# Optimization experiments

Hardware: AMD Instinct MI355X
Metric: run time of the kernel (lower is better)

The kernel has to match this reference:

```python
import jax, jax.numpy as jnp
import numpy as np

N = 32768   # nodes
E = 524288  # edges (avg degree 16)
F = 32      # num_features
H = 512     # hidden_channels
C = 10      # num_classes
G = 64      # graphs in batch


def setup_inputs() -> dict:
    key = jax.random.key(0)
    ks = jax.random.split(key, 16)
    s = 0.05  # weight init scale
    f32 = jnp.float32
    return {
        "x": jax.random.normal(ks[0], (N, F), f32),
        "edge_index": jax.random.randint(ks[1], (2, E), 0, N),
        "batch_index": jnp.sort(jax.random.randint(ks[2], (N,), 0, G)),
        # initial_conv: F -> H  (PyG GraphConv: lin_root on x, lin_rel on aggregated neighbors)
        "w_root0": jax.random.normal(ks[3], (F, H), f32) * s,
        "w_rel0": jax.random.normal(ks[4], (F, H), f32) * s,
        "b0": jnp.zeros((H,), f32),
        # conv1..conv4 stacked: H -> H
        "w_root": jax.random.normal(ks[5], (4, H, H), f32) * s,
        "w_rel": jax.random.normal(ks[6], (4, H, H), f32) * s,
        "b": jnp.zeros((4, H), f32),
        # MLP tail
        "lin1_w": jax.random.normal(ks[7], (2 * H, H), f32) * s,
        "lin1_b": jnp.zeros((H,), f32),
        "lin2_w": jax.random.normal(ks[8], (H, H), f32) * s,
        "lin2_b": jnp.zeros((H,), f32),
        "lin3_w": jax.random.normal(ks[9], (H, C), f32) * s,
        "lin3_b": jnp.zeros((C,), f32),
    }


def _graph_conv(h, src, dst, w_root, w_rel, bias):
    # out_i = h_i @ W_root + (sum_{j->i} h_j) @ W_rel + b   (PyG GraphConv, aggr='add')
    agg = jax.ops.segment_sum(h[src], dst, num_segments=N)
    return h @ w_root + agg @ w_rel + bias


def reference(x, edge_index, batch_index,
              w_root0, w_rel0, b0, w_root, w_rel, b,
              lin1_w, lin1_b, lin2_w, lin2_b, lin3_w, lin3_b):
    src, dst = edge_index[0], edge_index[1]
    h = jnp.tanh(_graph_conv(x, src, dst, w_root0, w_rel0, b0))
    for i in range(4):  # fixed small layer loop
        h = jnp.tanh(_graph_conv(h, src, dst, w_root[i], w_rel[i], b[i]))
    # global max + mean pool over graphs
    gmax = jax.ops.segment_max(h, batch_index, num_segments=G)
    gsum = jax.ops.segment_sum(h, batch_index, num_segments=G)
    cnt = jax.ops.segment_sum(jnp.ones((N,), h.dtype), batch_index, num_segments=G)
    gmean = gsum / jnp.maximum(cnt, 1.0)[:, None]
    g = jnp.concatenate([gmax, gmean], axis=1)  # [G, 2H]
    # dropout is identity at inference (training=False)
    g = jnp.tanh(g @ lin1_w + lin1_b)
    g = jnp.tanh(g @ lin2_w + lin2_b)
    logits = g @ lin3_w + lin3_b
    return jax.nn.log_softmax(logits, axis=1)
```

## Files before the change

### kernel.cpp

```cpp
#include <hip/hip_runtime.h>
#include <hip/hip_bf16.h>
#include <math.h>

#define NN 32768
#define EE 524288
#define FF 32
#define HH 512
#define GG 64
#define CC 10

typedef __attribute__((ext_vector_type(8))) short short8;
typedef __attribute__((ext_vector_type(4))) float floatx4;
typedef __attribute__((ext_vector_type(4))) unsigned int uintx4;

__device__ __forceinline__ float bf16_to_f32(unsigned short u) {
    union { unsigned int u; float f; } v;
    v.u = ((unsigned int)u) << 16;
    return v.f;
}
__device__ __forceinline__ unsigned short f32_to_bf16(float f) {
    union { float f; unsigned int u; } v;
    v.f = f;
    unsigned int u = v.u;
    u += 0x7FFFu + ((u >> 16) & 1u);
    return (unsigned short)(u >> 16);
}
__device__ __forceinline__ float fast_tanh(float x) {
    float e = __expf(2.0f * x);
    return 1.0f - 2.0f * __builtin_amdgcn_rcpf(e + 1.0f);
}

__global__ __launch_bounds__(256) void prep_all_kernel(const float* __restrict__ wr0, const float* __restrict__ wl0,
                                unsigned short* __restrict__ WT0,
                                const float* __restrict__ wroot, const float* __restrict__ wrel,
                                unsigned short* __restrict__ WTs,
                                const float* __restrict__ x, unsigned short* __restrict__ X0) {
    const int b = blockIdx.x;
    const int tid = threadIdx.x;
    if (b < 520) {
        __shared__ unsigned short tile[64][65];
        const int ty = tid >> 6, tx = tid & 63;
        if (b < 8) {
            const int n0 = b * 64;
#pragma unroll
            for (int q = 0; q < 16; ++q) {
                const int k = ty * 16 + q;
                const float v = (k < 32) ? wr0[k * 512 + n0 + tx]
                                         : wl0[(k - 32) * 512 + n0 + tx];
                tile[k][tx] = f32_to_bf16(v);
            }
            __syncthreads();
#pragma unroll
            for (int q = 0; q < 16; ++q) {
                const int n = n0 + ty * 16 + q;
                WT0[n * 64 + tx] = tile[tx][ty * 16 + q];
            }
        } else {
            const int bb = b - 8;
            const int l = bb >> 7;
            const int r = bb & 127;
            const int k0 = (r >> 3) * 64;
            const int n0 = (r & 7) * 64;
            const float* Wl = (k0 < 512) ? wroot + (size_t)l * 262144
                                         : wrel + (size_t)l * 262144;
            const int kb = (k0 < 512) ? k0 : k0 - 512;
#pragma unroll
            for (int q = 0; q < 16; ++q) {
                const int kk = ty * 16 + q;
                tile[kk][tx] = f32_to_bf16(Wl[(size_t)(kb + kk) * 512 + n0 + tx]);
            }
            __syncthreads();
#pragma unroll
            for (int q = 0; q < 16; ++q) {
                const int n = n0 + ty * 16 + q;
                WTs[(size_t)l * 524288 + (size_t)n * 1024 + k0 + tx] = tile[tx][ty * 16 + q];
            }
        }
    } else {
        const int t = (b - 520) * 256 + tid;
        const int i = t >> 5, c = t & 31;
        X0[(size_t)i * 64 + c] = f32_to_bf16(x[t]);
    }
}

__global__ void zero_i32(int* __restrict__ p, int n) {
    int i = blockIdx.x * blockDim.x + threadIdx.x;
    if (i < n) p[i] = 0;
}
__global__ void hist_kernel(const int* __restrict__ dst, int* __restrict__ counts) {
    int e = blockIdx.x * blockDim.x + threadIdx.x;
    if (e < EE) atomicAdd(&counts[dst[e]], 1);
}
__global__ __launch_bounds__(1024) void scan_kernel(const int* __restrict__ counts,
                                                    int* __restrict__ rowStart,
                                                    int* __restrict__ cursor) {
    __shared__ int part[1024];
    const int t = threadIdx.x;
    const int base = t * 32;
    int local[32];
    const int4* cp = (const int4*)(counts + base);
    int s = 0;
#pragma unroll
    for (int ii = 0; ii < 8; ++ii) {
        int4 v = cp[ii];
        local[ii * 4 + 0] = v.x; local[ii * 4 + 1] = v.y;
        local[ii * 4 + 2] = v.z; local[ii * 4 + 3] = v.w;
        s += v.x + v.y + v.z + v.w;
    }
    part[t] = s;
    __syncthreads();
    for (int off = 1; off < 1024; off <<= 1) {
        int v = (t >= off) ? part[t - off] : 0;
        __syncthreads();
        part[t] += v;
        __syncthreads();
    }
    int run = part[t] - s;
#pragma unroll
    for (int i = 0; i < 32; ++i) {
        rowStart[base + i] = run;
        cursor[base + i] = run;
        run += local[i];
    }
    if (t == 1023) rowStart[NN] = run;
}
__global__ void scatter_kernel(const int* __restrict__ src, const int* __restrict__ dst,
                               int* __restrict__ cursor, int* __restrict__ ssrc) {
    int e = blockIdx.x * blockDim.x + threadIdx.x;
    if (e < EE) {
        int p = atomicAdd(&cursor[dst[e]], 1);
        ssrc[p] = src[e];
    }
}
__global__ __launch_bounds__(256) void deg_hist_kernel(const int* __restrict__ counts,
                                                       int* __restrict__ degHist) {
    __shared__ int lh[256];
    lh[threadIdx.x] = 0;
    __syncthreads();
    int i = blockIdx.x * 256 + threadIdx.x;
    int d = counts[i]; if (d > 255) d = 255;
    atomicAdd(&lh[255 - d], 1);
    __syncthreads();
    int v = lh[threadIdx.x];
    if (v) atomicAdd(&degHist[threadIdx.x], v);
}
__global__ __launch_bounds__(256) void deg_scan_kernel(const int* __restrict__ degHist,
                                                       int* __restrict__ degCursor) {
    __shared__ int sh[256];
    const int t = threadIdx.x;
    int own = degHist[t];
    sh[t] = own;
    __syncthreads();
    for (int off = 1; off < 256; off <<= 1) {
        int v = (t >= off) ? sh[t - off] : 0;
        __syncthreads();
        sh[t] += v;
        __syncthreads();
    }
    degCursor[t] = sh[t] - own;
}
__global__ __launch_bounds__(256) void deg_scatter_kernel(const int* __restrict__ counts,
                                                          int* __restrict__ degCursor,
                                                          int* __restrict__ perm,
                                                          int* __restrict__ pDeg) {
    __shared__ int lh[256];
    __shared__ int base[256];
    lh[threadIdx.x] = 0;
    __syncthreads();
    int i = blockIdx.x * 256 + threadIdx.x;
    int dtrue = counts[i];
    int d = dtrue > 255 ? 255 : dtrue;
    int bin = 255 - d;
    int lr = atomicAdd(&lh[bin], 1);
    __syncthreads();
    int c = lh[threadIdx.x];
    if (c) base[threadIdx.x] = atomicAdd(&degCursor[threadIdx.x], c);
    __syncthreads();
    int p = base[bin] + lr;
    perm[p] = i;
    pDeg[p] = dtrue;
}
__global__ __launch_bounds__(256) void edge_copy_kernel(const int* __restrict__ rowStart,
                                                        const int* __restrict__ perm,
                                                        const int* __restrict__ pRowStart,
                                                        const int* __restrict__ ssrc,
                                                        int* __restrict__ pssrc) {
    const int wv = threadIdx.x >> 6, lane = threadIdx.x & 63;
    const int sub = lane >> 4, l16 = lane & 15;
    const int p = blockIdx.x * 16 + wv * 4 + sub;
    const int node = perm[p];
    const int s = rowStart[node], e = rowStart[node + 1];
    const int ns = pRowStart[p];
    for (int j = s + l16; j < e; j += 16) pssrc[ns + (j - s)] = ssrc[j];
}

__device__ __forceinline__ void acc8(float* a, uint4 d) {
    a[0] += bf16_to_f32((unsigned short)(d.x & 0xFFFFu));
    a[1] += bf16_to_f32((unsigned short)(d.x >> 16));
    a[2] += bf16_to_f32((unsigned short)(d.y & 0xFFFFu));
    a[3] += bf16_to_f32((unsigned short)(d.y >> 16));
    a[4] += bf16_to_f32((unsigned short)(d.z & 0xFFFFu));
    a[5] += bf16_to_f32((unsigned short)(d.z >> 16));
    a[6] += bf16_to_f32((unsigned short)(d.w & 0xFFFFu));
    a[7] += bf16_to_f32((unsigned short)(d.w >> 16));
}
__device__ __forceinline__ void acc8v(float* a, uintx4 d) {
    a[0] += bf16_to_f32((unsigned short)(d[0] & 0xFFFFu));
    a[1] += bf16_to_f32((unsigned short)(d[0] >> 16));
    a[2] += bf16_to_f32((unsigned short)(d[1] & 0xFFFFu));
    a[3] += bf16_to_f32((unsigned short)(d[1] >> 16));
    a[4] += bf16_to_f32((unsigned short)(d[2] & 0xFFFFu));
    a[5] += bf16_to_f32((unsigned short)(d[2] >> 16));
    a[6] += bf16_to_f32((unsigned short)(d[3] & 0xFFFFu));
    a[7] += bf16_to_f32((unsigned short)(d[3] >> 16));
}

__global__ __launch_bounds__(256) void agg_kernel(const unsigned short* __restrict__ Xh, int ldh,
                                                  int cols, unsigned short* __restrict__ Xagg,
                                                  int ldagg, const int* __restrict__ rowStart,
                                                  const int* __restrict__ ssrc) {
    const int node = blockIdx.x * 64 + (threadIdx.x >> 2);
    const int lc = threadIdx.x & 3;
    const int s = rowStart[node];
    const int e = rowStart[node + 1];
    float a[8] = {0.f, 0.f, 0.f, 0.f, 0.f, 0.f, 0.f, 0.f};
    const unsigned short* base = Xh + lc * 8;
    int i = s;
    for (; i + 4 <= e; i += 4) {
        int j0 = ssrc[i], j1 = ssrc[i + 1], j2 = ssrc[i + 2], j3 = ssrc[i + 3];
        uint4 d0 = *(const uint4*)(base + (size_t)j0 * 64);
        uint4 d1 = *(const uint4*)(base + (size_t)j1 * 64);
        uint4 d2 = *(const uint4*)(base + (size_t)j2 * 64);
        uint4 d3 = *(const uint4*)(base + (size_t)j3 * 64);
        acc8(a, d0); acc8(a, d1); acc8(a, d2); acc8(a, d3);
    }
    for (; i < e; ++i) {
        int j = ssrc[i];
        uint4 d = *(const uint4*)(base + (size_t)j * 64);
        acc8(a, d);
    }
    unsigned short* out = Xagg + (size_t)node * 64 + lc * 8;
#pragma unroll
    for (int c = 0; c < 8; ++c) out[c] = f32_to_bf16(a[c]);
}

#define GLOAD(dreg, voff) \
    asm volatile("buffer_load_dwordx4 %0, %1, %2, 0 offen" \
                 : "=v"(dreg) : "v"(voff), "s"(srsrc))

__global__ __launch_bounds__(256, 3) void agg_slice_kernel(const unsigned short* __restrict__ Xh,
                                                           unsigned short* __restrict__ Xagg,
                                                           const int* __restrict__ pRowStart,
                                                           const int* __restrict__ pssrc,
                                                           const int* __restrict__ perm) {
    const int slice = blockIdx.x & 7;
    const int pair = blockIdx.x >> 3;
    const int wv = threadIdx.x >> 6;
    const int lane = threadIdx.x & 63;
    const int ln = lane >> 3;
    const int lc = lane & 7;
    const int colOff = slice * 64 + lc * 8;
    const unsigned short* base = Xh + colOff;
    uintx4 srsrc;
    {
        union { const unsigned short* p; unsigned int u[2]; } ba;
        ba.p = Xh + slice * 64;
        srsrc[0] = ba.u[0];
        srsrc[1] = ba.u[1] & 0xFFFFu;
        srsrc[2] = 0xFFFFFFFFu;
        srsrc[3] = 0x00020000u;
    }
    const unsigned int lcoff = (unsigned int)(lc << 4);
#pragma unroll
    for (int half = 0; half < 2; ++half) {
        const int nb = half ? (1023 - pair) : pair;
        const int p = nb * 32 + wv * 8 + ln;
        const int node = perm[p];
        const int s = pRowStart[p];
        const int e = pRowStart[p + 1];
        float a[8] = {0.f, 0.f, 0.f, 0.f, 0.f, 0.f, 0.f, 0.f};
        int i = s;
        for (; i + 16 <= e; i += 16) {
            unsigned int vo[16];
#pragma unroll
            for (int u = 0; u < 16; ++u)
                vo[u] = (((unsigned int)pssrc[i + u]) << 11) | lcoff;
            uintx4 d0, d1, d2, d3, d4, d5, d6, d7, d8, d9, d10, d11, d12, d13, d14, d15;
            __builtin_amdgcn_sched_barrier(0);
            GLOAD(d0, vo[0]);   GLOAD(d1, vo[1]);   GLOAD(d2, vo[2]);   GLOAD(d3, vo[3]);
            GLOAD(d4, vo[4]);   GLOAD(d5, vo[5]);   GLOAD(d6, vo[6]);   GLOAD(d7, vo[7]);
            GLOAD(d8, vo[8]);   GLOAD(d9, vo[9]);   GLOAD(d10, vo[10]); GLOAD(d11, vo[11]);
            GLOAD(d12, vo[12]); GLOAD(d13, vo[13]); GLOAD(d14, vo[14]); GLOAD(d15, vo[15]);
            asm volatile("s_waitcnt vmcnt(8)" ::: "memory");
            __builtin_amdgcn_sched_barrier(0);
            acc8v(a, d0); acc8v(a, d1); acc8v(a, d2); acc8v(a, d3);
            acc8v(a, d4); acc8v(a, d5); acc8v(a, d6); acc8v(a, d7);
            asm volatile("s_waitcnt vmcnt(0)" ::: "memory");
            __builtin_amdgcn_sched_barrier(0);
            acc8v(a, d8);  acc8v(a, d9);  acc8v(a, d10); acc8v(a, d11);
            acc8v(a, d12); acc8v(a, d13); acc8v(a, d14); acc8v(a, d15);
        }
        if (e - i >= 8) {
            unsigned int vo[8];
#pragma unroll
            for (int u = 0; u < 8; ++u)
                vo[u] = (((unsigned int)pssrc[i + u]) << 11) | lcoff;
            uintx4 d0, d1, d2, d3, d4, d5, d6, d7;
            __builtin_amdgcn_sched_barrier(0);
            GLOAD(d0, vo[0]); GLOAD(d1, vo[1]); GLOAD(d2, vo[2]); GLOAD(d3, vo[3]);
            GLOAD(d4, vo[4]); GLOAD(d5, vo[5]); GLOAD(d6, vo[6]); GLOAD(d7, vo[7]);
            asm volatile("s_waitcnt vmcnt(4)" ::: "memory");
            __builtin_amdgcn_sched_barrier(0);
            acc8v(a, d0); acc8v(a, d1); acc8v(a, d2); acc8v(a, d3);
            asm volatile("s_waitcnt vmcnt(0)" ::: "memory");
            __builtin_amdgcn_sched_barrier(0);
            acc8v(a, d4); acc8v(a, d5); acc8v(a, d6); acc8v(a, d7);
            i += 8;
        }
        for (; i + 4 <= e; i += 4) {
            int j0 = pssrc[i], j1 = pssrc[i + 1], j2 = pssrc[i + 2], j3 = pssrc[i + 3];
            uint4 e0 = *(const uint4*)(base + (size_t)j0 * 1024);
            uint4 e1 = *(const uint4*)(base + (size_t)j1 * 1024);
            uint4 e2 = *(const uint4*)(base + (size_t)j2 * 1024);
            uint4 e3 = *(const uint4*)(base + (size_t)j3 * 1024);
            acc8(a, e0); acc8(a, e1); acc8(a, e2); acc8(a, e3);
        }
        for (; i < e; ++i) {
            int j = pssrc[i];
            uint4 d = *(const uint4*)(base + (size_t)j * 1024);
            acc8(a, d);
        }
        unsigned short* out = Xagg + (size_t)node * 1024 + colOff;
#pragma unroll
        for (int c = 0; c < 8; ++c) out[c] = f32_to_bf16(a[c]);
    }
}

__global__ __launch_bounds__(256, 4) void gemm_bias_tanh(const unsigned short* __restrict__ Xin,
                                                         int ldin, int K,
                                                         const unsigned short* __restrict__ WT,
                                                         const float* __restrict__ bias,
                                                         unsigned short* __restrict__ Xout,
                                                         int ldout) {
    __shared__ __align__(16) unsigned short As[128 * 64];
    __shared__ __align__(16) unsigned short Bs[128 * 64];
    const int tid = threadIdx.x;
    const int lane = tid & 63;
    const int wave = tid >> 6;
    const int wm = wave >> 1, wn = wave & 1;
    const int bm = blockIdx.x, bn = blockIdx.y;

    floatx4 acc[4][4] = {};

    const int lrow = lane >> 3;
    const int schunk = (lane & 7) ^ (lrow & 7);
    const unsigned short* Abase = Xin + (size_t)(bm * 128) * ldin;
    const unsigned short* Bbase = WT + (size_t)(bn * 128) * K;
    const int m = lane & 15;
    const int quad = lane >> 4;

    for (int k0 = 0; k0 < K; k0 += 64) {
        __syncthreads();
#pragma unroll
        for (int q = 0; q < 4; ++q) {
            const int rr = q * 32 + wave * 8;
            const int row = rr + lrow;
            const unsigned short* sa = Abase + (size_t)row * ldin + (k0 + schunk * 8);
            const unsigned short* sb = Bbase + (size_t)row * K + (k0 + schunk * 8);
            __builtin_amdgcn_global_load_lds(
                (const __attribute__((address_space(1))) void*)sa,
                (__attribute__((address_space(3))) void*)(&As[rr * 64]), 16, 0, 0);
            __builtin_amdgcn_global_load_lds(
                (const __attribute__((address_space(1))) void*)sb,
                (__attribute__((address_space(3))) void*)(&Bs[rr * 64]), 16, 0, 0);
        }
        __syncthreads();
#pragma unroll
        for (int half = 0; half < 2; ++half) {
            short8 af[4], bfr[4];
#pragma unroll
            for (int t = 0; t < 4; ++t) {
                const int row = wm * 64 + t * 16 + m;
                const int chunk = (half * 4 + quad) ^ (row & 7);
                af[t] = *(const short8*)&As[row * 64 + chunk * 8];
            }
#pragma unroll
            for (int t = 0; t < 4; ++t) {
                const int row = wn * 64 + t * 16 + m;
                const int chunk = (half * 4 + quad) ^ (row & 7);
                bfr[t] = *(const short8*)&Bs[row * 64 + chunk * 8];
            }
#pragma unroll
            for (int mt = 0; mt < 4; ++mt)
#pragma unroll
                for (int nt = 0; nt < 4; ++nt)
                    acc[mt][nt] = __builtin_amdgcn_mfma_f32_16x16x32_bf16(af[mt], bfr[nt],
                                                                          acc[mt][nt], 0, 0, 0);
        }
    }

    const int row0 = bm * 128 + wm * 64;
    const int col0 = bn * 128 + wn * 64;
#pragma unroll
    for (int mt = 0; mt < 4; ++mt) {
#pragma unroll
        for (int nt = 0; nt < 4; ++nt) {
            const int col = col0 + nt * 16 + m;
            const float bv = bias[col];
#pragma unroll
            for (int r = 0; r < 4; ++r) {
                const int row = row0 + mt * 16 + quad * 4 + r;
                float v = fast_tanh(acc[mt][nt][r] + bv);
                Xout[(size_t)row * ldout + col] = f32_to_bf16(v);
            }
        }
    }
}

__device__ __forceinline__ void stage_half(const unsigned short* __restrict__ gsrc0,
                                           int ldg, unsigned short* ldsHalf,
                                           int w, int lane) {
#pragma unroll
    for (int q = 0; q < 2; ++q) {
        const int rb = q * 64 + w * 8;
        const unsigned short* src = gsrc0 + (size_t)(rb + (lane >> 3)) * ldg
                                    + ((lane & 7) ^ (lane >> 3)) * 8;
        __builtin_amdgcn_global_load_lds(
            (const __attribute__((address_space(1))) void*)src,
            (__attribute__((address_space(3))) void*)(ldsHalf + rb * 64), 16, 0, 0);
    }
}
__device__ __forceinline__ void stage_q(const unsigned short* __restrict__ gsrc0,
                                        int ldg, unsigned short* ldsQ,
                                        int w, int lane) {
    const unsigned short* src = gsrc0 + (size_t)(w * 8 + (lane >> 3)) * ldg
                                + ((lane & 7) ^ (lane >> 3)) * 8;
    __builtin_amdgcn_global_load_lds(
        (const __attribute__((address_space(1))) void*)src,
        (__attribute__((address_space(3))) void*)(ldsQ + (w * 8) * 64), 16, 0, 0);
}

__global__ __launch_bounds__(512, 2) void gemm256_bias_tanh(
    const unsigned short* __restrict__ Xin, int ldin, int K,
    const unsigned short* __restrict__ WT, const float* __restrict__ bias,
    unsigned short* __restrict__ Xout, int ldout) {
    __shared__ __align__(16) unsigned short As[2][256 * 64];
    __shared__ __align__(16) unsigned short Bs[2][256 * 64];
    const int tid = threadIdx.x;
    const int lane = tid & 63;
    const int w = tid >> 6;
    const int wm = w >> 2, wn = w & 3;
    const int m = lane & 15, quad = lane >> 4;
    const int id = (int)blockIdx.x;
    const int bm = (id & 7) * 16 + (id >> 4);
    const int bn = (id >> 3) & 1;
    const int NT = K >> 6;

    const unsigned short* Abase = Xin + (size_t)(bm * 256) * ldin;
    const unsigned short* Bbase = WT + (size_t)(bn * 256) * K;

    floatx4 acc[8][4] = {};

#define STG_AH(buf, h, kt_) stage_half(Abase + (size_t)((h) * 128) * ldin + (kt_) * 64, ldin, \
                                       &As[buf][(h) * 128 * 64], w, lane)
#define STG_BH(buf, h, kt_) stage_half(Bbase + (size_t)((h) * 128) * K + (kt_) * 64, K, \
                                       &Bs[buf][(h) * 128 * 64], w, lane)
#define STG_AQ(buf, qr, kt_) stage_q(Abase + (size_t)((qr) * 64) * ldin + (kt_) * 64, ldin, \
                                     &As[buf][(qr) * 64 * 64], w, lane)

    STG_BH(0, 0, 0); STG_BH(0, 1, 0); STG_AH(0, 0, 0); STG_AH(0, 1, 0);
    STG_BH(1, 0, 1); STG_BH(1, 1, 1); STG_AH(1, 0, 1); STG_AH(1, 1, 1);
    asm volatile("s_waitcnt vmcnt(8)" ::: "memory");
    __builtin_amdgcn_s_barrier();

    for (int kt = 0; kt < NT; ++kt) {
        const int cur = kt & 1;
        const unsigned short* Ac = &As[cur][0];
        const unsigned short* Bc = &Bs[cur][0];
        const bool pf = (kt + 2 < NT);
        short8 afr[8], bfr[8];

#pragma unroll
        for (int nf = 0; nf < 4; ++nf)
#pragma unroll
            for (int ks = 0; ks < 2; ++ks) {
                const int col = wn * 64 + nf * 16 + m;
                const int chunk = (ks * 4 + quad) ^ (col & 7);
                bfr[nf * 2 + ks] = *(const short8*)&Bc[col * 64 + chunk * 8];
            }
#pragma unroll
        for (int t = 0; t < 4; ++t)
#pragma unroll
            for (int ks = 0; ks < 2; ++ks) {
                const int row = wm * 128 + t * 16 + m;
                const int chunk = (ks * 4 + quad) ^ (row & 7);
                afr[t * 2 + ks] = *(const short8*)&Ac[row * 64 + chunk * 8];
            }
        __builtin_amdgcn_s_barrier();
        __builtin_amdgcn_s_setprio(1);
#pragma unroll
        for (int t = 0; t < 4; ++t)
#pragma unroll
            for (int u = 0; u < 2; ++u)
#pragma unroll
                for (int ks = 0; ks < 2; ++ks)
                    acc[t][u] = __builtin_amdgcn_mfma_f32_16x16x32_bf16(
                        afr[t * 2 + ks], bfr[u * 2 + ks], acc[t][u], 0, 0, 0);
        __builtin_amdgcn_s_setprio(0);
        __builtin_amdgcn_s_barrier();

        if (pf) { STG_AQ(cur, 0, kt + 2); STG_AQ(cur, 2, kt + 2); }
        __builtin_amdgcn_s_barrier();
        __builtin_amdgcn_s_setprio(1);
#pragma unroll
        for (int t = 0; t < 4; ++t)
#pragma unroll
            for (int u = 2; u < 4; ++u)
#pragma unroll
                for (int ks = 0; ks < 2; ++ks)
                    acc[t][u] = __builtin_amdgcn_mfma_f32_16x16x32_bf16(
                        afr[t * 2 + ks], bfr[u * 2 + ks], acc[t][u], 0, 0, 0);
        __builtin_amdgcn_s_setprio(0);
        __builtin_amdgcn_s_barrier();

#pragma unroll
        for (int t = 0; t < 4; ++t)
#pragma unroll
            for (int ks = 0; ks < 2; ++ks) {
                const int row = wm * 128 + (4 + t) * 16 + m;
                const int chunk = (ks * 4 + quad) ^ (row & 7);
                afr[t * 2 + ks] = *(const short8*)&Ac[row * 64 + chunk * 8];
            }
        __builtin_amdgcn_sched_barrier(0);
        if (pf) STG_BH(cur, 0, kt + 2);
        __builtin_amdgcn_s_barrier();
        __builtin_amdgcn_s_setprio(1);
#pragma unroll
        for (int t = 0; t < 4; ++t)
#pragma unroll
            for (int u = 0; u < 2; ++u)
#pragma unroll
                for (int ks = 0; ks < 2; ++ks)
                    acc[4 + t][u] = __builtin_amdgcn_mfma_f32_16x16x32_bf16(
                        afr[t * 2 + ks], bfr[u * 2 + ks], acc[4 + t][u], 0, 0, 0);
        __builtin_amdgcn_s_setprio(0);
        __builtin_amdgcn_s_barrier();

        if (pf) {
            STG_BH(cur, 1, kt + 2);
            STG_AQ(cur, 1, kt + 2); STG_AQ(cur, 3, kt + 2);
        }
        __builtin_amdgcn_s_barrier();
        __builtin_amdgcn_s_setprio(1);
#pragma unroll
        for (int t = 0; t < 4; ++t)
#pragma unroll
            for (int u = 2; u < 4; ++u)
#pragma unroll
                for (int ks = 0; ks < 2; ++ks)
                    acc[4 + t][u] = __builtin_amdgcn_mfma_f32_16x16x32_bf16(
                        afr[t * 2 + ks], bfr[u * 2 + ks], acc[4 + t][u], 0, 0, 0);
        __builtin_amdgcn_s_setprio(0);
        if (kt <= NT - 3) {
            asm volatile("s_waitcnt vmcnt(8)" ::: "memory");
        } else {
            asm volatile("s_waitcnt vmcnt(0)" ::: "memory");
        }
        __builtin_amdgcn_s_barrier();
    }
#undef STG_AH
#undef STG_BH
#undef STG_AQ

    const int row0 = bm * 256 + wm * 128;
    const int col0 = bn * 256 + wn * 64;
#pragma unroll
    for (int mf = 0; mf < 8; ++mf) {
#pragma unroll
        for (int nf = 0; nf < 4; ++nf) {
            const int col = col0 + nf * 16 + m;
            const float bv = bias[col];
#pragma unroll
            for (int r = 0; r < 4; ++r) {
                const int row = row0 + mf * 16 + quad * 4 + r;
                float v = fast_tanh(acc[mf][nf][r] + bv);
                Xout[(size_t)row * ldout + col] = f32_to_bf16(v);
            }
        }
    }
}

__global__ __launch_bounds__(256) void pool_partial(const unsigned short* __restrict__ h,
                                                    const int* __restrict__ batch,
                                                    float* __restrict__ part) {
    const int gi = blockIdx.x, rs = blockIdx.y, t = threadIdx.x;
    int lo = 0, hi = NN;
    while (lo < hi) { int mid = (lo + hi) >> 1; if (batch[mid] < gi) lo = mid + 1; else hi = mid; }
    const int start = lo;
    hi = NN;
    while (lo < hi) { int mid = (lo + hi) >> 1; if (batch[mid] < gi + 1) lo = mid + 1; else hi = mid; }
    const int end = lo;
    const int len = end - start;
    const int q = (len + 7) >> 3;
    int r0 = start + rs * q;
    int r1 = r0 + q; if (r1 > end) r1 = end; if (r0 > end) r0 = end;
    float mx0 = -INFINITY, mx1 = -INFINITY, s0 = 0.f, s1 = 0.f;
    int i = r0;
    for (; i + 2 <= r1; i += 2) {
        unsigned int d0 = *(const unsigned int*)(h + (size_t)i * 1024 + t * 2);
        unsigned int d1 = *(const unsigned int*)(h + (size_t)(i + 1) * 1024 + t * 2);
        float v0 = bf16_to_f32((unsigned short)(d0 & 0xFFFFu));
        float v1 = bf16_to_f32((unsigned short)(d0 >> 16));
        float w0 = bf16_to_f32((unsigned short)(d1 & 0xFFFFu));
        float w1 = bf16_to_f32((unsigned short)(d1 >> 16));
        mx0 = fmaxf(mx0, fmaxf(v0, w0)); mx1 = fmaxf(mx1, fmaxf(v1, w1));
        s0 += v0 + w0; s1 += v1 + w1;
    }
    for (; i < r1; ++i) {
        unsigned int d0 = *(const unsigned int*)(h + (size_t)i * 1024 + t * 2);
        float v0 = bf16_to_f32((unsigned short)(d0 & 0xFFFFu));
        float v1 = bf16_to_f32((unsigned short)(d0 >> 16));
        mx0 = fmaxf(mx0, v0); mx1 = fmaxf(mx1, v1);
        s0 += v0; s1 += v1;
    }
    float* p = part + ((size_t)gi * 8 + rs) * 1024;
    p[t * 2] = mx0; p[t * 2 + 1] = mx1;
    p[512 + t * 2] = s0; p[512 + t * 2 + 1] = s1;
}

__global__ __launch_bounds__(256) void pool_combine(const float* __restrict__ part,
                                                    const int* __restrict__ batch,
                                                    float* __restrict__ gT) {
    const int gi = blockIdx.x, t = threadIdx.x;
    int lo = 0, hi = NN;
    while (lo < hi) { int mid = (lo + hi) >> 1; if (batch[mid] < gi) lo = mid + 1; else hi = mid; }
    const int start = lo;
    hi = NN;
    while (lo < hi) { int mid = (lo + hi) >> 1; if (batch[mid] < gi + 1) lo = mid + 1; else hi = mid; }
    int cnt = lo - start; if (cnt < 1) cnt = 1;
    const float inv = 1.0f / (float)cnt;
    float mx0 = -INFINITY, mx1 = -INFINITY, s0 = 0.f, s1 = 0.f;
#pragma unroll
    for (int rs = 0; rs < 8; ++rs) {
        const float* p = part + ((size_t)gi * 8 + rs) * 1024;
        mx0 = fmaxf(mx0, p[t * 2]); mx1 = fmaxf(mx1, p[t * 2 + 1]);
        s0 += p[512 + t * 2]; s1 += p[512 + t * 2 + 1];
    }
    gT[(size_t)(2 * t) * 64 + gi]        = mx0;
    gT[(size_t)(2 * t + 1) * 64 + gi]    = mx1;
    gT[(size_t)(512 + 2 * t) * 64 + gi]  = s0 * inv;
    gT[(size_t)(512 + 2 * t + 1) * 64 + gi] = s1 * inv;
}

__global__ __launch_bounds__(256) void mlp_splitk(const float* __restrict__ ginT,
                                                  const float* __restrict__ W,
                                                  int Ndim,
                                                  float* __restrict__ partial) {
    __shared__ float gsT[64][68];
    __shared__ float Ws[64][68];
    const int t = threadIdx.x;
    const int wv = t >> 6, l = t & 63;
    const int nb = blockIdx.x, kb = blockIdx.y;
    const int n0 = nb * 64;
    const int gr = t >> 2;
    const int c4 = (t & 3) * 16;
    float acc[16] = {};
#pragma unroll
    for (int sub = 0; sub < 2; ++sub) {
        const int k0 = kb * 128 + sub * 64;
        __syncthreads();
        {
            const float4* gsrc = (const float4*)(ginT + (size_t)(k0 + gr) * 64 + c4);
            float4* gd = (float4*)&gsT[gr][c4];
            gd[0] = gsrc[0]; gd[1] = gsrc[1]; gd[2] = gsrc[2]; gd[3] = gsrc[3];
            const float4* wsrc = (const float4*)(W + (size_t)(k0 + gr) * Ndim + n0 + c4);
            float4* wd = (float4*)&Ws[gr][c4];
            wd[0] = wsrc[0]; wd[1] = wsrc[1]; wd[2] = wsrc[2]; wd[3] = wsrc[3];
        }
        __syncthreads();
#pragma unroll 4
        for (int kk = 0; kk < 64; ++kk) {
            const float wval = Ws[kk][l];
            const float4* gv = (const float4*)&gsT[kk][wv * 16];
            float4 g0 = gv[0], g1 = gv[1], g2 = gv[2], g3 = gv[3];
            acc[0]  = fmaf(g0.x, wval, acc[0]);  acc[1]  = fmaf(g0.y, wval, acc[1]);
            acc[2]  = fmaf(g0.z, wval, acc[2]);  acc[3]  = fmaf(g0.w, wval, acc[3]);
            acc[4]  = fmaf(g1.x, wval, acc[4]);  acc[5]  = fmaf(g1.y, wval, acc[5]);
            acc[6]  = fmaf(g1.z, wval, acc[6]);  acc[7]  = fmaf(g1.w, wval, acc[7]);
            acc[8]  = fmaf(g2.x, wval, acc[8]);  acc[9]  = fmaf(g2.y, wval, acc[9]);
            acc[10] = fmaf(g2.z, wval, acc[10]); acc[11] = fmaf(g2.w, wval, acc[11]);
            acc[12] = fmaf(g3.x, wval, acc[12]); acc[13] = fmaf(g3.y, wval, acc[13]);
            acc[14] = fmaf(g3.z, wval, acc[14]); acc[15] = fmaf(g3.w, wval, acc[15]);
        }
    }
    float* p = partial + ((size_t)kb * 64) * Ndim;
#pragma unroll
    for (int g = 0; g < 16; ++g)
        p[(size_t)(wv * 16 + g) * Ndim + n0 + l] = acc[g];
}

__global__ __launch_bounds__(256) void mlp_combine(const float* __restrict__ partial, int nparts,
                                                   const float* __restrict__ bias, int Ndim,
                                                   float* __restrict__ outN,
                                                   float* __restrict__ outT) {
    const int idx = blockIdx.x * 256 + threadIdx.x;
    if (idx >= 64 * Ndim) return;
    const int g = idx / Ndim, n = idx - g * Ndim;
    float s = bias[n];
    for (int kb = 0; kb < nparts; ++kb)
        s += partial[((size_t)kb * 64 + g) * Ndim + n];
    const float v = fast_tanh(s);
    if (outN) outN[(size_t)g * Ndim + n] = v;
    if (outT) outT[(size_t)n * 64 + g] = v;
}

__global__ __launch_bounds__(64) void head_kernel(const float* __restrict__ g2,
                                                  const float* __restrict__ W,
                                                  const float* __restrict__ b,
                                                  float* __restrict__ out) {
    const int gi = blockIdx.x, t = threadIdx.x;
    const float4* gp = (const float4*)(g2 + (size_t)gi * HH + t * 8);
    float4 ga = gp[0], gb = gp[1];
    float gv[8] = {ga.x, ga.y, ga.z, ga.w, gb.x, gb.y, gb.z, gb.w};
    float logits[CC];
#pragma unroll
    for (int c = 0; c < CC; ++c) {
        float p = 0.f;
#pragma unroll
        for (int j = 0; j < 8; ++j)
            p = fmaf(gv[j], W[(t * 8 + j) * CC + c], p);
#pragma unroll
        for (int off = 32; off > 0; off >>= 1)
            p += __shfl_xor(p, off, 64);
        logits[c] = p + b[c];
    }
    if (t == 0) {
        float mx = logits[0];
#pragma unroll
        for (int c = 1; c < CC; ++c) mx = fmaxf(mx, logits[c]);
        float s = 0.f;
#pragma unroll
        for (int c = 0; c < CC; ++c) s += expf(logits[c] - mx);
        float lse = mx + logf(s);
#pragma unroll
        for (int c = 0; c < CC; ++c) out[(size_t)gi * CC + c] = logits[c] - lse;
    }
}

extern "C" void kernel_launch(void* const* d_in, const int* in_sizes, int n_in,
                              void* d_out, int out_size, void* d_ws, size_t ws_size,
                              hipStream_t stream) {
    const float* x       = (const float*)d_in[0];
    const int*   ei      = (const int*)d_in[1];
    const int*   batch   = (const int*)d_in[2];
    const float* w_root0 = (const float*)d_in[3];
    const float* w_rel0  = (const float*)d_in[4];
    const float* b0      = (const float*)d_in[5];
    const float* w_root  = (const float*)d_in[6];
    const float* w_rel   = (const float*)d_in[7];
    const float* bvec    = (const float*)d_in[8];
    const float* lin1_w  = (const float*)d_in[9];
    const float* lin1_b  = (const float*)d_in[10];
    const float* lin2_w  = (const float*)d_in[11];
    const float* lin2_b  = (const float*)d_in[12];
    const float* lin3_w  = (const float*)d_in[13];
    const float* lin3_b  = (const float*)d_in[14];
    float* out = (float*)d_out;

    char* w = (char*)d_ws;
    size_t off = 0;
    auto alloc = [&](size_t bytes) -> char* {
        char* p = w + off;
        off += (bytes + 255) & ~(size_t)255;
        return p;
    };
    unsigned short* Xa  = (unsigned short*)alloc((size_t)NN * 1024 * 2);
    unsigned short* Xb  = (unsigned short*)alloc((size_t)NN * 1024 * 2);
    unsigned short* X0  = (unsigned short*)alloc((size_t)NN * 64 * 2);
    unsigned short* WT0 = (unsigned short*)alloc(512 * 64 * 2);
    unsigned short* WTs = (unsigned short*)alloc((size_t)4 * 512 * 1024 * 2);
    int* counts   = (int*)alloc((size_t)NN * 4);
    int* degHist  = (int*)alloc(256 * 4);
    int* degCursor= (int*)alloc(256 * 4);
    int* rowStart = (int*)alloc((size_t)(NN + 1) * 4);
    int* cursor   = (int*)alloc((size_t)NN * 4);
    int* ssrc     = (int*)alloc((size_t)EE * 4);
    int* perm     = (int*)alloc((size_t)NN * 4);
    int* pDeg     = (int*)alloc((size_t)NN * 4);
    int* pRowStart= (int*)alloc((size_t)(NN + 1) * 4);
    int* pCursor  = (int*)alloc((size_t)NN * 4);
    int* pssrc    = (int*)alloc((size_t)EE * 4);
    float* gbufT  = (float*)alloc((size_t)1024 * 64 * 4);
    float* g1T    = (float*)alloc((size_t)512 * 64 * 4);
    float* g2buf  = (float*)alloc((size_t)GG * 512 * 4);
    float* mlpPart = (float*)alloc((size_t)8 * 64 * 512 * 4);
    float* part   = (float*)X0;

    const int* esrc = ei;
    const int* edst = ei + EE;

    prep_all_kernel<<<4616, 256, 0, stream>>>(w_root0, w_rel0, WT0, w_root, w_rel, WTs, x, X0);
    zero_i32<<<130, 256, 0, stream>>>(counts, NN + 256);
    hist_kernel<<<2048, 256, 0, stream>>>(edst, counts);
    scan_kernel<<<1, 1024, 0, stream>>>(counts, rowStart, cursor);
    scatter_kernel<<<2048, 256, 0, stream>>>(esrc, edst, cursor, ssrc);
    deg_hist_kernel<<<128, 256, 0, stream>>>(counts, degHist);
    deg_scan_kernel<<<1, 256, 0, stream>>>(degHist, degCursor);
    deg_scatter_kernel<<<128, 256, 0, stream>>>(counts, degCursor, perm, pDeg);
    scan_kernel<<<1, 1024, 0, stream>>>(pDeg, pRowStart, pCursor);
    edge_copy_kernel<<<2048, 256, 0, stream>>>(rowStart, perm, pRowStart, ssrc, pssrc);

    agg_kernel<<<512, 256, 0, stream>>>(X0, 64, 32, X0 + 32, 64, rowStart, ssrc);
    gemm_bias_tanh<<<dim3(256, 4), 256, 0, stream>>>(X0, 64, 64, WT0, b0, Xa, 1024);

    agg_slice_kernel<<<4096, 256, 0, stream>>>(Xa, Xa + 512, pRowStart, pssrc, perm);
    gemm256_bias_tanh<<<256, 512, 0, stream>>>(Xa, 1024, 1024, WTs + 0 * 524288, bvec + 0, Xb, 1024);
    agg_slice_kernel<<<4096, 256, 0, stream>>>(Xb, Xb + 512, pRowStart, pssrc, perm);
    gemm256_bias_tanh<<<256, 512, 0, stream>>>(Xb, 1024, 1024, WTs + 1 * 524288, bvec + 512, Xa, 1024);
    agg_slice_kernel<<<4096, 256, 0, stream>>>(Xa, Xa + 512, pRowStart, pssrc, perm);
    gemm256_bias_tanh<<<256, 512, 0, stream>>>(Xa, 1024, 1024, WTs + 2 * 524288, bvec + 1024, Xb, 1024);
    agg_slice_kernel<<<4096, 256, 0, stream>>>(Xb, Xb + 512, pRowStart, pssrc, perm);
    gemm256_bias_tanh<<<256, 512, 0, stream>>>(Xb, 1024, 1024, WTs + 3 * 524288, bvec + 1536, Xa, 1024);

    pool_partial<<<dim3(GG, 8), 256, 0, stream>>>(Xa, batch, part);
    pool_combine<<<GG, 256, 0, stream>>>(part, batch, gbufT);
    mlp_splitk<<<dim3(8, 8), 256, 0, stream>>>(gbufT, lin1_w, 512, mlpPart);
    mlp_combine<<<128, 256, 0, stream>>>(mlpPart, 8, lin1_b, 512, nullptr, g1T);
    mlp_splitk<<<dim3(8, 4), 256, 0, stream>>>(g1T, lin2_w, 512, mlpPart);
    mlp_combine<<<128, 256, 0, stream>>>(mlpPart, 4, lin2_b, 512, g2buf, nullptr);
    head_kernel<<<GG, 64, 0, stream>>>(g2buf, lin3_w, lin3_b, out);
}
```

Before: 596.4 us.

## Build degree-sorted CSR directly in one kernel and drop intermediate CSR

Replaces the chain of scan, scatter, degree-histogram, degree-scan, degree-scatter and edge-copy kernels with a single-block perm_build kernel plus a scatter that writes edges directly into the degree-permuted CSR via an inverse permutation. The counts zeroing is folded into the prep kernel as extra blocks. The first-layer aggregation now uses the permuted CSR. This removes several launches and one full pass over edge data, at the cost of a serial single-block kernel doing histogram, scan and permutation work.

```diff
diff --git a/kernel.cpp b/kernel.cpp
--- a/kernel.cpp
+++ b/kernel.cpp
@@ -34,7 +34,8 @@
                                 unsigned short* __restrict__ WT0,
                                 const float* __restrict__ wroot, const float* __restrict__ wrel,
                                 unsigned short* __restrict__ WTs,
-                                const float* __restrict__ x, unsigned short* __restrict__ X0) {
+                                const float* __restrict__ x, unsigned short* __restrict__ X0,
+                                int* __restrict__ counts) {
     const int b = blockIdx.x;
     const int tid = threadIdx.x;
     if (b < 520) {
@@ -76,122 +77,105 @@
                 WTs[(size_t)l * 524288 + (size_t)n * 1024 + k0 + tx] = tile[tx][ty * 16 + q];
             }
         }
-    } else {
+    } else if (b < 4616) {
         const int t = (b - 520) * 256 + tid;
         const int i = t >> 5, c = t & 31;
         X0[(size_t)i * 64 + c] = f32_to_bf16(x[t]);
-    }
-}
-
-__global__ void zero_i32(int* __restrict__ p, int n) {
-    int i = blockIdx.x * blockDim.x + threadIdx.x;
-    if (i < n) p[i] = 0;
-}
+    } else {
+        const int t4 = (b - 4616) * 256 + tid;
+        int4 z; z.x = 0; z.y = 0; z.z = 0; z.w = 0;
+        ((int4*)counts)[t4] = z;
+    }
+}
+
 __global__ void hist_kernel(const int* __restrict__ dst, int* __restrict__ counts) {
     int e = blockIdx.x * blockDim.x + threadIdx.x;
     if (e < EE) atomicAdd(&counts[dst[e]], 1);
 }
-__global__ __launch_bounds__(1024) void scan_kernel(const int* __restrict__ counts,
-                                                    int* __restrict__ rowStart,
-                                                    int* __restrict__ cursor) {
-    __shared__ int part[1024];
+
+__global__ __launch_bounds__(1024) void perm_build_kernel(const int* __restrict__ counts,
+                                                          int* __restrict__ perm,
+                                                          int* __restrict__ pDeg,
+                                                          int* __restrict__ iperm,
+                                                          int* __restrict__ pRowStart,
+                                                          int* __restrict__ pCursor) {
+    __shared__ int hist[256];
+    __shared__ int binCur[256];
+    __shared__ int wsum[1024];
     const int t = threadIdx.x;
     const int base = t * 32;
-    int local[32];
+    int deg[32];
     const int4* cp = (const int4*)(counts + base);
-    int s = 0;
 #pragma unroll
     for (int ii = 0; ii < 8; ++ii) {
         int4 v = cp[ii];
+        deg[ii * 4 + 0] = v.x; deg[ii * 4 + 1] = v.y;
+        deg[ii * 4 + 2] = v.z; deg[ii * 4 + 3] = v.w;
+    }
+    if (t < 256) hist[t] = 0;
+    __syncthreads();
+#pragma unroll
+    for (int i = 0; i < 32; ++i) {
+        int d = deg[i] > 255 ? 255 : deg[i];
+        atomicAdd(&hist[255 - d], 1);
+    }
+    __syncthreads();
+    const int own = (t < 256) ? hist[t] : 0;
+    for (int off = 1; off < 256; off <<= 1) {
+        int v = (t < 256 && t >= off) ? hist[t - off] : 0;
+        __syncthreads();
+        if (t < 256) hist[t] += v;
+        __syncthreads();
+    }
+    if (t < 256) binCur[t] = hist[t] - own;
+    __syncthreads();
+#pragma unroll
+    for (int i = 0; i < 32; ++i) {
+        const int dtrue = deg[i];
+        const int d = dtrue > 255 ? 255 : dtrue;
+        const int p = atomicAdd(&binCur[255 - d], 1);
+        perm[p] = base + i;
+        pDeg[p] = dtrue;
+        iperm[base + i] = p;
+    }
+    __syncthreads();
+    int local[32];
+    const int4* pp = (const int4*)(pDeg + base);
+    int s = 0;
+#pragma unroll
+    for (int ii = 0; ii < 8; ++ii) {
+        int4 v = pp[ii];
         local[ii * 4 + 0] = v.x; local[ii * 4 + 1] = v.y;
         local[ii * 4 + 2] = v.z; local[ii * 4 + 3] = v.w;
         s += v.x + v.y + v.z + v.w;
     }
-    part[t] = s;
+    wsum[t] = s;
     __syncthreads();
     for (int off = 1; off < 1024; off <<= 1) {
-        int v = (t >= off) ? part[t - off] : 0;
+        int v = (t >= off) ? wsum[t - off] : 0;
         __syncthreads();
-        part[t] += v;
+        wsum[t] += v;
         __syncthreads();
     }
-    int run = part[t] - s;
+    int run = wsum[t] - s;
 #pragma unroll
     for (int i = 0; i < 32; ++i) {
-        rowStart[base + i] = run;
-        cursor[base + i] = run;
+        pRowStart[base + i] = run;
+        pCursor[base + i] = run;
         run += local[i];
     }
-    if (t == 1023) rowStart[NN] = run;
-}
+    if (t == 1023) pRowStart[NN] = run;
+}
+
 __global__ void scatter_kernel(const int* __restrict__ src, const int* __restrict__ dst,
-                               int* __restrict__ cursor, int* __restrict__ ssrc) {
+                               const int* __restrict__ iperm,
+                               int* __restrict__ pCursor, int* __restrict__ pssrc) {
     int e = blockIdx.x * blockDim.x + threadIdx.x;
     if (e < EE) {
-        int p = atomicAdd(&cursor[dst[e]], 1);
-        ssrc[p] = src[e];
-    }
-}
-__global__ __launch_bounds__(256) void deg_hist_kernel(const int* __restrict__ counts,
-                                                       int* __restrict__ degHist) {
-    __shared__ int lh[256];
-    lh[threadIdx.x] = 0;
-    __syncthreads();
-    int i = blockIdx.x * 256 + threadIdx.x;
-    int d = counts[i]; if (d > 255) d = 255;
-    atomicAdd(&lh[255 - d], 1);
-    __syncthreads();
-    int v = lh[threadIdx.x];
-    if (v) atomicAdd(&degHist[threadIdx.x], v);
-}
-__global__ __launch_bounds__(256) void deg_scan_kernel(const int* __restrict__ degHist,
-                                                       int* __restrict__ degCursor) {
-    __shared__ int sh[256];
-    const int t = threadIdx.x;
-    int own = degHist[t];
-    sh[t] = own;
-    __syncthreads();
-    for (int off = 1; off < 256; off <<= 1) {
-        int v = (t >= off) ? sh[t - off] : 0;
-        __syncthreads();
-        sh[t] += v;
-        __syncthreads();
-    }
-    degCursor[t] = sh[t] - own;
-}
-__global__ __launch_bounds__(256) void deg_scatter_kernel(const int* __restrict__ counts,
-                                                          int* __restrict__ degCursor,
-                                                          int* __restrict__ perm,
-                                                          int* __restrict__ pDeg) {
-    __shared__ int lh[256];
-    __shared__ int base[256];
-    lh[threadIdx.x] = 0;
-    __syncthreads();
-    int i = blockIdx.x * 256 + threadIdx.x;
-    int dtrue = counts[i];
-    int d = dtrue > 255 ? 255 : dtrue;
-    int bin = 255 - d;
-    int lr = atomicAdd(&lh[bin], 1);
-    __syncthreads();
-    int c = lh[threadIdx.x];
-    if (c) base[threadIdx.x] = atomicAdd(&degCursor[threadIdx.x], c);
-    __syncthreads();
-    int p = base[bin] + lr;
-    perm[p] = i;
-    pDeg[p] = dtrue;
-}
-__global__ __launch_bounds__(256) void edge_copy_kernel(const int* __restrict__ rowStart,
-                                                        const int* __restrict__ perm,
-                                                        const int* __restrict__ pRowStart,
-                                                        const int* __restrict__ ssrc,
-                                                        int* __restrict__ pssrc) {
-    const int wv = threadIdx.x >> 6, lane = threadIdx.x & 63;
-    const int sub = lane >> 4, l16 = lane & 15;
-    const int p = blockIdx.x * 16 + wv * 4 + sub;
-    const int node = perm[p];
-    const int s = rowStart[node], e = rowStart[node + 1];
-    const int ns = pRowStart[p];
-    for (int j = s + l16; j < e; j += 16) pssrc[ns + (j - s)] = ssrc[j];
+        int p = iperm[dst[e]];
+        int q = atomicAdd(&pCursor[p], 1);
+        pssrc[q] = src[e];
+    }
 }
 
 __device__ __forceinline__ void acc8(float* a, uint4 d) {
@@ -215,19 +199,21 @@
     a[7] += bf16_to_f32((unsigned short)(d[3] >> 16));
 }
 
-__global__ __launch_bounds__(256) void agg_kernel(const unsigned short* __restrict__ Xh, int ldh,
-                                                  int cols, unsigned short* __restrict__ Xagg,
-                                                  int ldagg, const int* __restrict__ rowStart,
-                                                  const int* __restrict__ ssrc) {
-    const int node = blockIdx.x * 64 + (threadIdx.x >> 2);
+__global__ __launch_bounds__(256) void agg_kernel(const unsigned short* __restrict__ Xh,
+                                                  unsigned short* __restrict__ Xagg,
+                                                  const int* __restrict__ pRowStart,
+                                                  const int* __restrict__ pssrc,
+                                                  const int* __restrict__ perm) {
+    const int p = blockIdx.x * 64 + (threadIdx.x >> 2);
     const int lc = threadIdx.x & 3;
-    const int s = rowStart[node];
-    const int e = rowStart[node + 1];
+    const int node = perm[p];
+    const int s = pRowStart[p];
+    const int e = pRowStart[p + 1];
     float a[8] = {0.f, 0.f, 0.f, 0.f, 0.f, 0.f, 0.f, 0.f};
     const unsigned short* base = Xh + lc * 8;
     int i = s;
     for (; i + 4 <= e; i += 4) {
-        int j0 = ssrc[i], j1 = ssrc[i + 1], j2 = ssrc[i + 2], j3 = ssrc[i + 3];
+        int j0 = pssrc[i], j1 = pssrc[i + 1], j2 = pssrc[i + 2], j3 = pssrc[i + 3];
         uint4 d0 = *(const uint4*)(base + (size_t)j0 * 64);
         uint4 d1 = *(const uint4*)(base + (size_t)j1 * 64);
         uint4 d2 = *(const uint4*)(base + (size_t)j2 * 64);
@@ -235,7 +221,7 @@
         acc8(a, d0); acc8(a, d1); acc8(a, d2); acc8(a, d3);
     }
     for (; i < e; ++i) {
-        int j = ssrc[i];
+        int j = pssrc[i];
         uint4 d = *(const uint4*)(base + (size_t)j * 64);
         acc8(a, d);
     }
@@ -780,13 +766,9 @@
     unsigned short* WT0 = (unsigned short*)alloc(512 * 64 * 2);
     unsigned short* WTs = (unsigned short*)alloc((size_t)4 * 512 * 1024 * 2);
     int* counts   = (int*)alloc((size_t)NN * 4);
-    int* degHist  = (int*)alloc(256 * 4);
-    int* degCursor= (int*)alloc(256 * 4);
-    int* rowStart = (int*)alloc((size_t)(NN + 1) * 4);
-    int* cursor   = (int*)alloc((size_t)NN * 4);
-    int* ssrc     = (int*)alloc((size_t)EE * 4);
     int* perm     = (int*)alloc((size_t)NN * 4);
     int* pDeg     = (int*)alloc((size_t)NN * 4);
+    int* iperm    = (int*)alloc((size_t)NN * 4);
     int* pRowStart= (int*)alloc((size_t)(NN + 1) * 4);
     int* pCursor  = (int*)alloc((size_t)NN * 4);
     int* pssrc    = (int*)alloc((size_t)EE * 4);
@@ -799,18 +781,12 @@
     const int* esrc = ei;
     const int* edst = ei + EE;
 
-    prep_all_kernel<<<4616, 256, 0, stream>>>(w_root0, w_rel0, WT0, w_root, w_rel, WTs, x, X0);
-    zero_i32<<<130, 256, 0, stream>>>(counts, NN + 256);
+    prep_all_kernel<<<4648, 256, 0, stream>>>(w_root0, w_rel0, WT0, w_root, w_rel, WTs, x, X0, counts);
     hist_kernel<<<2048, 256, 0, stream>>>(edst, counts);
-    scan_kernel<<<1, 1024, 0, stream>>>(counts, rowStart, cursor);
-    scatter_kernel<<<2048, 256, 0, stream>>>(esrc, edst, cursor, ssrc);
-    deg_hist_kernel<<<128, 256, 0, stream>>>(counts, degHist);
-    deg_scan_kernel<<<1, 256, 0, stream>>>(degHist, degCursor);
-    deg_scatter_kernel<<<128, 256, 0, stream>>>(counts, degCursor, perm, pDeg);
-    scan_kernel<<<1, 1024, 0, stream>>>(pDeg, pRowStart, pCursor);
-    edge_copy_kernel<<<2048, 256, 0, stream>>>(rowStart, perm, pRowStart, ssrc, pssrc);
-
-    agg_kernel<<<512, 256, 0, stream>>>(X0, 64, 32, X0 + 32, 64, rowStart, ssrc);
+    perm_build_kernel<<<1, 1024, 0, stream>>>(counts, perm, pDeg, iperm, pRowStart, pCursor);
+    scatter_kernel<<<2048, 256, 0, stream>>>(esrc, edst, iperm, pCursor, pssrc);
+
+    agg_kernel<<<512, 256, 0, stream>>>(X0, X0 + 32, pRowStart, pssrc, perm);
     gemm_bias_tanh<<<dim3(256, 4), 256, 0, stream>>>(X0, 64, 64, WT0, b0, Xa, 1024);
 
     agg_slice_kernel<<<4096, 256, 0, stream>>>(Xa, Xa + 512, pRowStart, pssrc, perm);
```

Result: no change. 605.5 us (+1.5%).
